# Performance work log

Hardware: AMD Instinct MI355X
Metric: run time of the kernel (lower is better)

Reference implementation:

```python
import jax, jax.numpy as jnp
import numpy as np

B, S, D = 8, 1024, 1152
H = 16
HD = D // H
HID = int(D * 4.0)
LN_EPS = 1e-5


def layer_norm(x, w, b):
    m = jnp.mean(x, axis=-1, keepdims=True)
    v = jnp.mean(jnp.square(x - m), axis=-1, keepdims=True)
    return (x - m) * jax.lax.rsqrt(v + LN_EPS) * w + b


def modulate(x, shift, scale):
    # shift/scale: [B, D] broadcast over seq
    return x * (1.0 + scale[:, None, :]) + shift[:, None, :]


def setup_inputs() -> dict:
    key = jax.random.key(0)
    ks = jax.random.split(key, 16)
    s = 0.02
    return {
        "x": jax.random.normal(ks[0], (B, S, D), jnp.float32),
        "c": jax.random.normal(ks[1], (B, D), jnp.float32),
        "ln1_w": jnp.ones((D,), jnp.float32),
        "ln1_b": jnp.zeros((D,), jnp.float32),
        "wq": jax.random.normal(ks[2], (D, D), jnp.float32) * s,
        "wk": jax.random.normal(ks[3], (D, D), jnp.float32) * s,
        "wv": jax.random.normal(ks[4], (D, D), jnp.float32) * s,
        "wo": jax.random.normal(ks[5], (D, D), jnp.float32) * s,
        "wo_b": jnp.zeros((D,), jnp.float32),
        "ln2_w": jnp.ones((D,), jnp.float32),
        "ln2_b": jnp.zeros((D,), jnp.float32),
        "fc1_w": jax.random.normal(ks[6], (D, HID), jnp.float32) * s,
        "fc1_b": jnp.zeros((HID,), jnp.float32),
        "fc2_w": jax.random.normal(ks[7], (HID, D), jnp.float32) * s,
        "fc2_b": jnp.zeros((D,), jnp.float32),
        "ada_w": jax.random.normal(ks[8], (D, 6 * D), jnp.float32) * s,
        "ada_b": jnp.zeros((6 * D,), jnp.float32),
    }


def attention(x, wq, wk, wv, wo, wo_b):
    b, s, d = x.shape
    q = (x @ wq).reshape(b, s, H, HD).transpose(0, 2, 1, 3)  # [B,H,S,hd]
    k = (x @ wk).reshape(b, s, H, HD).transpose(0, 2, 1, 3)
    v = (x @ wv).reshape(b, s, H, HD).transpose(0, 2, 1, 3)
    scale = 1.0 / np.sqrt(HD).astype(np.float32)
    att = jnp.einsum("bhqd,bhkd->bhqk", q, k) * scale
    att = jax.nn.softmax(att, axis=-1)
    out = jnp.einsum("bhqk,bhkd->bhqd", att, v)
    out = out.transpose(0, 2, 1, 3).reshape(b, s, d)
    return out @ wo + wo_b


def reference(x, c, ln1_w, ln1_b, wq, wk, wv, wo, wo_b, ln2_w, ln2_b,
              fc1_w, fc1_b, fc2_w, fc2_b, ada_w, ada_b):
    mod = jax.nn.silu(c) @ ada_w + ada_b  # [B, 6D]
    sh_msa, sc_msa, g_msa, sh_mlp, sc_mlp, g_mlp = jnp.split(mod, 6, axis=1)
    h = modulate(layer_norm(x, ln1_w, ln1_b), sh_msa, sc_msa)
    x = x + g_msa[:, None, :] * attention(h, wq, wk, wv, wo, wo_b)
    h = modulate(layer_norm(x, ln2_w, ln2_b), sh_mlp, sc_mlp)
    h = jax.nn.gelu(h @ fc1_w + fc1_b, approximate=False) @ fc2_w + fc2_b
    x = x + g_mlp[:, None, :] * h
    return x
```

## Files before the change

kernel.cpp:

```cpp
#include <hip/hip_runtime.h>
#include <hip/hip_bf16.h>


typedef unsigned short u16;
typedef unsigned int u32;
typedef __attribute__((ext_vector_type(8))) short bf16x8;
typedef __attribute__((ext_vector_type(4))) float f32x4;
typedef __attribute__((ext_vector_type(16))) float f32x16;

#define MFMA16(a, b, c) __builtin_amdgcn_mfma_f32_16x16x32_bf16((a), (b), (c), 0, 0, 0)
#define MFMA32(a, b, c) __builtin_amdgcn_mfma_f32_32x32x16_bf16((a), (b), (c), 0, 0, 0)

__device__ __forceinline__ u16 f2bf(float f) {
  __hip_bfloat16 h = __float2bfloat16(f);
  return __builtin_bit_cast(u16, h);
}

__device__ __forceinline__ float bf2f(u16 u) {
  u32 v = ((u32)u) << 16;
  return __builtin_bit_cast(float, v);
}

__device__ __forceinline__ void gload16(const u16* g, u16* l) {
  __builtin_amdgcn_global_load_lds(
      (const __attribute__((address_space(1))) unsigned int*)(const void*)g,
      (__attribute__((address_space(3))) unsigned int*)(void*)l, 16, 0, 0);
}

__global__ __launch_bounds__(256) void k_modproj1(const float* __restrict__ cc,
                                                  const float* __restrict__ aw,
                                                  float* __restrict__ partial) {
  __shared__ float lc[8][144];
  int kc = blockIdx.y;
  for (int i = threadIdx.x; i < 1152; i += 256) {
    int b = i / 144, k = i % 144;
    float v = cc[b * 1152 + kc * 144 + k];
    lc[b][k] = v / (1.f + __expf(-v));
  }
  __syncthreads();
  int j = blockIdx.x * 256 + threadIdx.x;
  float acc[8] = {0, 0, 0, 0, 0, 0, 0, 0};
  for (int k = 0; k < 144; ++k) {
    float w = aw[(size_t)(kc * 144 + k) * 6912 + j];
    #pragma unroll
    for (int b = 0; b < 8; ++b) acc[b] += lc[b][k] * w;
  }
  #pragma unroll
  for (int b = 0; b < 8; ++b) partial[((size_t)kc * 8 + b) * 6912 + j] = acc[b];
}

__global__ __launch_bounds__(256) void k_modproj2(const float* __restrict__ partial,
                                                  const float* __restrict__ ab,
                                                  float* __restrict__ mo) {
  int j = blockIdx.x * 256 + threadIdx.x;
  float bias = ab[j];
  #pragma unroll
  for (int b = 0; b < 8; ++b) {
    float s = 0.f;
    #pragma unroll
    for (int kc = 0; kc < 8; ++kc) s += partial[((size_t)kc * 8 + b) * 6912 + j];
    mo[(size_t)b * 6912 + j] = s + bias;
  }
}

__global__ __launch_bounds__(256) void k_tcvt(const float* __restrict__ in, u16* __restrict__ out,
                                              int K, int N) {
  __shared__ float t[32][33];
  int tx = threadIdx.x & 31, ty = threadIdx.x >> 5;
  size_t bx = (size_t)blockIdx.x * 32, by = (size_t)blockIdx.y * 32;
  #pragma unroll
  for (int i = 0; i < 4; ++i) t[ty + 8 * i][tx] = in[(by + ty + 8 * i) * N + bx + tx];
  __syncthreads();
  #pragma unroll
  for (int i = 0; i < 4; ++i) out[(bx + ty + 8 * i) * K + by + tx] = f2bf(t[tx][ty + 8 * i]);
}

__global__ __launch_bounds__(256) void k_lnmod(const float* __restrict__ xin,
                                               const float* __restrict__ w,
                                               const float* __restrict__ bs,
                                               const float* __restrict__ mo,
                                               int sh_off, int sc_off, u16* __restrict__ o) {
  int row = blockIdx.x;
  int b = row >> 10;
  int tid = threadIdx.x;
  const float4* x4 = (const float4*)(xin + (size_t)row * 1152);
  float4 v0 = x4[tid];
  float4 v1 = make_float4(0.f, 0.f, 0.f, 0.f);
  if (tid < 32) v1 = x4[256 + tid];
  float s = v0.x + v0.y + v0.z + v0.w + v1.x + v1.y + v1.z + v1.w;
  float sq = v0.x * v0.x + v0.y * v0.y + v0.z * v0.z + v0.w * v0.w +
             v1.x * v1.x + v1.y * v1.y + v1.z * v1.z + v1.w * v1.w;
  #pragma unroll
  for (int d = 32; d > 0; d >>= 1) { s += __shfl_down(s, d); sq += __shfl_down(sq, d); }
  __shared__ float ps[4], pq[4];
  int wid = tid >> 6, lane = tid & 63;
  if (lane == 0) { ps[wid] = s; pq[wid] = sq; }
  __syncthreads();
  float S = ps[0] + ps[1] + ps[2] + ps[3];
  float SQ = pq[0] + pq[1] + pq[2] + pq[3];
  float mean = S * (1.f / 1152.f);
  float var = SQ * (1.f / 1152.f) - mean * mean;
  float rs = rsqrtf(var + 1e-5f);
  const float* shp = mo + (size_t)b * 6912 + sh_off;
  const float* scp = mo + (size_t)b * 6912 + sc_off;
  u16* orow = o + (size_t)row * 1152;
  {
    int col = 4 * tid;
    ushort4 u; float y;
    y = (v0.x - mean) * rs * w[col + 0] + bs[col + 0]; u.x = f2bf(y * (1.f + scp[col + 0]) + shp[col + 0]);
    y = (v0.y - mean) * rs * w[col + 1] + bs[col + 1]; u.y = f2bf(y * (1.f + scp[col + 1]) + shp[col + 1]);
    y = (v0.z - mean) * rs * w[col + 2] + bs[col + 2]; u.z = f2bf(y * (1.f + scp[col + 2]) + shp[col + 2]);
    y = (v0.w - mean) * rs * w[col + 3] + bs[col + 3]; u.w = f2bf(y * (1.f + scp[col + 3]) + shp[col + 3]);
    *(ushort4*)&orow[col] = u;
  }
  if (tid < 32) {
    int col = 1024 + 4 * tid;
    ushort4 u; float y;
    y = (v1.x - mean) * rs * w[col + 0] + bs[col + 0]; u.x = f2bf(y * (1.f + scp[col + 0]) + shp[col + 0]);
    y = (v1.y - mean) * rs * w[col + 1] + bs[col + 1]; u.y = f2bf(y * (1.f + scp[col + 1]) + shp[col + 1]);
    y = (v1.z - mean) * rs * w[col + 2] + bs[col + 2]; u.z = f2bf(y * (1.f + scp[col + 2]) + shp[col + 2]);
    y = (v1.w - mean) * rs * w[col + 3] + bs[col + 3]; u.w = f2bf(y * (1.f + scp[col + 3]) + shp[col + 3]);
    *(ushort4*)&orow[col] = u;
  }
}

template <int EPI>
__global__ __launch_bounds__(512, 2) void k_gemm8p(const u16* __restrict__ A,
                                                   const u16* __restrict__ Bt,
                                                   int Kst, int klen,
                                                   u16* __restrict__ Cb,
                                                   const float* __restrict__ bias,
                                                   u16* __restrict__ vt) {
  const int tid = threadIdx.x;
  const int w = tid >> 6, lane = tid & 63;
  const int wm = w >> 2, wn = w & 3;
  const int l31 = lane & 31, hi = lane >> 5;

  const int nwg = gridDim.x * gridDim.y;
  const int id = blockIdx.y * gridDim.x + blockIdx.x;
  const int swz = (id & 7) * (nwg >> 3) + (id >> 3);
  const int tM = (swz / gridDim.x) * 256, tN = (swz % gridDim.x) * 256;
  const int koff = blockIdx.z * klen;

  __shared__ u16 lA[2][2][256 * 32];
  __shared__ u16 lB[2][2][256 * 32];
  f32x16 acc[4][2];
  #pragma unroll
  for (int m = 0; m < 4; ++m)
    #pragma unroll
    for (int n = 0; n < 2; ++n)
      #pragma unroll
      for (int r = 0; r < 16; ++r) acc[m][n][r] = 0.f;

  const int lrow = lane >> 2, lseg = lane & 3;
  const int fl = (lrow & 3) ^ ((lrow >> 2) & 3);
  const u16* gA = A + (size_t)(tM + w * 32 + lrow) * Kst + (lseg ^ fl) * 8 + koff;
  const u16* gB = Bt + (size_t)(tN + w * 32 + lrow) * Kst + (lseg ^ fl) * 8 + koff;
  const size_t rstep = (size_t)16 * Kst;
  const int wo0 = (w * 32) * 32, wo1 = (w * 32 + 16) * 32;
  const int fr = (l31 & 3) ^ ((l31 >> 2) & 3);
  const int c0 = (hi ^ fr) * 8;
  const int c1 = ((hi ^ fr) ^ 2) * 8;
  const int arow = (wm * 128 + l31) * 32;
  const int brow = (wn * 64 + l31) * 32;

#define SA(BUF, KH, KO)                                       \
  do {                                                        \
    gload16(gA + (KO), &lA[BUF][KH][wo0]);                    \
    gload16(gA + rstep + (KO), &lA[BUF][KH][wo1]);            \
  } while (0)
#define SB(BUF, KH, KO)                                       \
  do {                                                        \
    gload16(gB + (KO), &lB[BUF][KH][wo0]);                    \
    gload16(gB + rstep + (KO), &lB[BUF][KH][wo1]);            \
  } while (0)
#define VM(Nst) asm volatile("s_waitcnt vmcnt(" #Nst ")" ::: "memory")

#define PHASE(CB, KH, PM, STAGE_STMT)                                            \
  do {                                                                           \
    __builtin_amdgcn_s_barrier();                                                \
    __builtin_amdgcn_sched_barrier(0);                                           \
    bf16x8 a0_ = *(const bf16x8*)&lA[CB][KH][arow + (2 * (PM)) * 1024 + c0];     \
    bf16x8 a1_ = *(const bf16x8*)&lA[CB][KH][arow + (2 * (PM)) * 1024 + c1];     \
    bf16x8 a2_ = *(const bf16x8*)&lA[CB][KH][arow + (2 * (PM) + 1) * 1024 + c0]; \
    bf16x8 a3_ = *(const bf16x8*)&lA[CB][KH][arow + (2 * (PM) + 1) * 1024 + c1]; \
    bf16x8 b0_ = *(const bf16x8*)&lB[CB][KH][brow + c0];                         \
    bf16x8 b1_ = *(const bf16x8*)&lB[CB][KH][brow + c1];                         \
    bf16x8 b2_ = *(const bf16x8*)&lB[CB][KH][brow + 1024 + c0];                  \
    bf16x8 b3_ = *(const bf16x8*)&lB[CB][KH][brow + 1024 + c1];                  \
    STAGE_STMT;                                                                  \
    asm volatile("s_waitcnt lgkmcnt(0)" ::: "memory");                           \
    __builtin_amdgcn_sched_barrier(0);                                           \
    __builtin_amdgcn_s_setprio(1);                                               \
    acc[2 * (PM)][0]     = MFMA32(a0_, b0_, acc[2 * (PM)][0]);                   \
    acc[2 * (PM)][1]     = MFMA32(a0_, b2_, acc[2 * (PM)][1]);                   \
    acc[2 * (PM) + 1][0] = MFMA32(a2_, b0_, acc[2 * (PM) + 1][0]);               \
    acc[2 * (PM) + 1][1] = MFMA32(a2_, b2_, acc[2 * (PM) + 1][1]);               \
    acc[2 * (PM)][0]     = MFMA32(a1_, b1_, acc[2 * (PM)][0]);                   \
    acc[2 * (PM)][1]     = MFMA32(a1_, b3_, acc[2 * (PM)][1]);                   \
    acc[2 * (PM) + 1][0] = MFMA32(a3_, b1_, acc[2 * (PM) + 1][0]);               \
    acc[2 * (PM) + 1][1] = MFMA32(a3_, b3_, acc[2 * (PM) + 1][1]);               \
    __builtin_amdgcn_s_setprio(0);                                               \
  } while (0)

  const int NIT = klen >> 7;
  SA(0, 0, 0); SB(0, 0, 0); SA(0, 1, 32); SB(0, 1, 32); SA(1, 0, 64);
  for (int it = 0; it < NIT - 1; ++it) {
    const int kb = it * 128;
    VM(6); PHASE(0, 0, 0, SB(1, 0, kb + 64));
           PHASE(0, 0, 1, SA(1, 1, kb + 96));
    VM(6); PHASE(0, 1, 0, SB(1, 1, kb + 96));
           PHASE(0, 1, 1, SA(0, 0, kb + 128));
    VM(6); PHASE(1, 0, 0, SB(0, 0, kb + 128));
           PHASE(1, 0, 1, SA(0, 1, kb + 160));
    VM(6); PHASE(1, 1, 0, SB(0, 1, kb + 160));
           PHASE(1, 1, 1, SA(1, 0, kb + 192));
  }
  {
    const int kb = (NIT - 1) * 128;
    VM(6); PHASE(0, 0, 0, SB(1, 0, kb + 64));
           PHASE(0, 0, 1, SA(1, 1, kb + 96));
    VM(6); PHASE(0, 1, 0, SB(1, 1, kb + 96));
           PHASE(0, 1, 1, (void)0);
    VM(4); PHASE(1, 0, 0, (void)0);
           PHASE(1, 0, 1, (void)0);
    VM(0); PHASE(1, 1, 0, (void)0);
           PHASE(1, 1, 1, (void)0);
  }
#undef SA
#undef SB
#undef VM
#undef PHASE

  #pragma unroll
  for (int m = 0; m < 4; ++m)
    #pragma unroll
    for (int n = 0; n < 2; ++n) {
      int gcol = tN + wn * 64 + n * 32 + l31;
      #pragma unroll
      for (int q = 0; q < 4; ++q) {
        int grow0 = tM + wm * 128 + m * 32 + hi * 4 + q * 8;
        if (EPI == 3) {
          if (gcol < 2304) {
            #pragma unroll
            for (int r = 0; r < 4; ++r)
              Cb[(size_t)(grow0 + r) * 3456 + gcol] = f2bf(acc[m][n][q * 4 + r]);
          } else if (gcol < 3456) {
            int qq = gcol - 2304;
            int hh = qq / 72;
            int d = qq - hh * 72;
            int bb = grow0 >> 10, sl = grow0 & 1023;
            ushort4 u;
            u.x = f2bf(acc[m][n][q * 4 + 0]); u.y = f2bf(acc[m][n][q * 4 + 1]);
            u.z = f2bf(acc[m][n][q * 4 + 2]); u.w = f2bf(acc[m][n][q * 4 + 3]);
            *(ushort4*)&vt[(((size_t)bb * 16 + hh) * 72 + d) * 1024 + sl] = u;
          }
        } else if (EPI == 5) {
          if (gcol < 1152) {
            u16* Po = Cb + (size_t)blockIdx.z * 9437184ull;
            #pragma unroll
            for (int r = 0; r < 4; ++r)
              Po[(size_t)(grow0 + r) * 1152 + gcol] = f2bf(acc[m][n][q * 4 + r]);
          }
        } else {
          const int NC = gridDim.x * 256;
          float bi = bias[gcol];
          #pragma unroll
          for (int r = 0; r < 4; ++r) {
            float z = acc[m][n][q * 4 + r] + bi;
            float z2 = z * z;
            float u = z * __fmaf_rn(z2, -0.0713548162f, -1.5957691216f);
            float e = __expf(u);
            Cb[(size_t)(grow0 + r) * NC + gcol] = f2bf(z * __builtin_amdgcn_rcpf(1.f + e));
          }
        }
      }
    }
}

template <int EPI>
__global__ __launch_bounds__(256) void k_gemm(const u16* __restrict__ A, const u16* __restrict__ Bt,
                                              int Kst, int klen, u16* __restrict__ Cb,
                                              float* __restrict__ Cf,
                                              const float* __restrict__ bias,
                                              const float* __restrict__ res,
                                              const float* __restrict__ mo, int goff,
                                              u16* __restrict__ vt) {
  const int tid = threadIdx.x;
  const int w = tid >> 6, lane = tid & 63;
  const int wr = w >> 1, wc = w & 1;
  const int l31 = lane & 31, hi = lane >> 5;

  const int nwg = gridDim.x * gridDim.y;
  const int id = blockIdx.y * gridDim.x + blockIdx.x;
  const int swz = (id & 7) * (nwg >> 3) + (id >> 3);
  const int tM = (swz / gridDim.x) * 128, tN = (swz % gridDim.x) * 128;
  const int N = gridDim.x * 128;
  const int koff = blockIdx.z * klen;

  __shared__ u16 lA[3][128 * 32];
  __shared__ u16 lB[3][128 * 32];
  f32x16 acc[2][2];
  #pragma unroll
  for (int m = 0; m < 2; ++m)
    #pragma unroll
    for (int n = 0; n < 2; ++n)
      #pragma unroll
      for (int r = 0; r < 16; ++r) acc[m][n][r] = 0.f;

  const int lrow = lane >> 2, lseg = lane & 3;
  const int fl = (lrow & 3) ^ ((lrow >> 2) & 3);
  const u16* gA = A + (size_t)(tM + w * 32 + lrow) * Kst + (lseg ^ fl) * 8 + koff;
  const u16* gB = Bt + (size_t)(tN + w * 32 + lrow) * Kst + (lseg ^ fl) * 8 + koff;
  const size_t rstep = (size_t)16 * Kst;
  const int wo0 = (w * 32) * 32, wo1 = (w * 32 + 16) * 32;
  const int fr = (l31 & 3) ^ ((l31 >> 2) & 3);
  const int c0 = (hi ^ fr) * 8;
  const int c1 = ((hi ^ fr) ^ 2) * 8;
  const int arow = (wr * 64 + l31) * 32;
  const int brow = (wc * 64 + l31) * 32;

#define STAGE(buf, ks)                        \
  do {                                        \
    gload16(gA + (ks), lA[buf] + wo0);        \
    gload16(gA + rstep + (ks), lA[buf] + wo1);\
    gload16(gB + (ks), lB[buf] + wo0);        \
    gload16(gB + rstep + (ks), lB[buf] + wo1);\
  } while (0)

#define COMPUTE(buf)                                                            \
  do {                                                                          \
    bf16x8 a00 = *(const bf16x8*)&lA[buf][arow + c0];                           \
    bf16x8 a01 = *(const bf16x8*)&lA[buf][arow + c1];                           \
    bf16x8 a10 = *(const bf16x8*)&lA[buf][arow + 1024 + c0];                    \
    bf16x8 a11 = *(const bf16x8*)&lA[buf][arow + 1024 + c1];                    \
    bf16x8 b00 = *(const bf16x8*)&lB[buf][brow + c0];                           \
    bf16x8 b01 = *(const bf16x8*)&lB[buf][brow + c1];                           \
    bf16x8 b10 = *(const bf16x8*)&lB[buf][brow + 1024 + c0];                    \
    bf16x8 b11 = *(const bf16x8*)&lB[buf][brow + 1024 + c1];                    \
    __builtin_amdgcn_s_setprio(1);                                              \
    acc[0][0] = MFMA32(a00, b00, acc[0][0]);                                    \
    acc[0][1] = MFMA32(a00, b10, acc[0][1]);                                    \
    acc[1][0] = MFMA32(a10, b00, acc[1][0]);                                    \
    acc[1][1] = MFMA32(a10, b10, acc[1][1]);                                    \
    acc[0][0] = MFMA32(a01, b01, acc[0][0]);                                    \
    acc[0][1] = MFMA32(a01, b11, acc[0][1]);                                    \
    acc[1][0] = MFMA32(a11, b01, acc[1][0]);                                    \
    acc[1][1] = MFMA32(a11, b11, acc[1][1]);                                    \
    __builtin_amdgcn_s_setprio(0);                                              \
  } while (0)

#define WAITBAR(Nst)                                          \
  do {                                                        \
    asm volatile("s_waitcnt vmcnt(" #Nst ")" ::: "memory");   \
    __builtin_amdgcn_s_barrier();                             \
    __builtin_amdgcn_sched_barrier(0);                        \
  } while (0)

  const int nt = klen >> 5;
  STAGE(0, 0);
  STAGE(1, 32);
  int ks = 64;
  for (int g = 0; g < nt / 3 - 1; ++g) {
    WAITBAR(4); STAGE(2, ks);      COMPUTE(0);
    WAITBAR(4); STAGE(0, ks + 32); COMPUTE(1);
    WAITBAR(4); STAGE(1, ks + 64); COMPUTE(2);
    ks += 96;
  }
  WAITBAR(4); STAGE(2, ks); COMPUTE(0);
  WAITBAR(4); COMPUTE(1);
  WAITBAR(0); COMPUTE(2);
#undef STAGE
#undef COMPUTE
#undef WAITBAR

  #pragma unroll
  for (int m = 0; m < 2; ++m)
    #pragma unroll
    for (int n = 0; n < 2; ++n) {
      int gcol = tN + wc * 64 + n * 32 + l31;
      #pragma unroll
      for (int q = 0; q < 4; ++q) {
        int grow0 = tM + wr * 64 + m * 32 + hi * 4 + q * 8;
        float g = mo[(size_t)(grow0 >> 10) * 6912 + goff + gcol];
        float bi = bias[gcol];
        #pragma unroll
        for (int r = 0; r < 4; ++r) {
          size_t idx = (size_t)(grow0 + r) * N + gcol;
          Cf[idx] = res[idx] + g * (acc[m][n][q * 4 + r] + bi);
        }
      }
    }
}

__global__ __launch_bounds__(256) void k_fc2red(const u16* __restrict__ p,
                                                const float* __restrict__ x1,
                                                const float* __restrict__ bias,
                                                const float* __restrict__ mo,
                                                float* __restrict__ out) {
  size_t i = ((size_t)blockIdx.x * 256 + threadIdx.x) * 4;
  int row = (int)(i / 1152);
  int col = (int)(i - (size_t)row * 1152);
  int b = row >> 10;
  ushort4 a0 = *(const ushort4*)(p + i);
  ushort4 a1 = *(const ushort4*)(p + 9437184ull + i);
  ushort4 a2 = *(const ushort4*)(p + 18874368ull + i);
  float4 r = *(const float4*)(x1 + i);
  const float* gp = mo + (size_t)b * 6912 + 5760 + col;
  const float* bp = bias + col;
  float4 o;
  o.x = r.x + gp[0] * (bf2f(a0.x) + bf2f(a1.x) + bf2f(a2.x) + bp[0]);
  o.y = r.y + gp[1] * (bf2f(a0.y) + bf2f(a1.y) + bf2f(a2.y) + bp[1]);
  o.z = r.z + gp[2] * (bf2f(a0.z) + bf2f(a1.z) + bf2f(a2.z) + bp[2]);
  o.w = r.w + gp[3] * (bf2f(a0.w) + bf2f(a1.w) + bf2f(a2.w) + bp[3]);
  *(float4*)(out + i) = o;
}

__global__ __launch_bounds__(256) void k_attn(const u16* __restrict__ QKV, const u16* __restrict__ Vt,
                                              u16* __restrict__ O) {
  const int tid = threadIdx.x;
  const int w = tid >> 6, lane = tid & 63;
  const int lr = lane & 15, kg = lane >> 4;
  int bx = blockIdx.x;
  bx = (bx & 7) * 256 + (bx >> 3);
  const int qt = bx & 15, h = (bx >> 4) & 15, b = bx >> 8;

  __shared__ u16 lQ[64][104];
  __shared__ u16 lK[64][104];
  __shared__ u16 lVt[80][72];
  __shared__ u16 lPt[4][16][72];

  const size_t qkbase = (size_t)b * 1024 * 3456 + (size_t)h * 72;
  const u16* Qg = QKV + qkbase;
  const u16* Kg = QKV + qkbase + 1152;
  const u16* Vg = Vt + ((size_t)(b * 16 + h) * 72) * 1024;

  const uint4 z4 = make_uint4(0, 0, 0, 0);
  for (int L = tid; L < 192; L += 256) {
    int r = L / 3, s = L - (L / 3) * 3;
    *(uint4*)&lQ[r][72 + s * 8] = z4;
    *(uint4*)&lK[r][72 + s * 8] = z4;
  }
  for (int L = tid; L < 72; L += 256) {
    int r = L / 9, s = L - (L / 9) * 9;
    *(uint4*)&lVt[72 + r][s * 8] = z4;
  }
  {
    int L = tid; int r = L / 9, s = L - r * 9;
    *(uint4*)&lQ[r][s * 8] = *(const uint4*)(Qg + (size_t)(qt * 64 + r) * 3456 + s * 8);
    L = tid + 256; r = L / 9; s = L - r * 9;
    *(uint4*)&lQ[r][s * 8] = *(const uint4*)(Qg + (size_t)(qt * 64 + r) * 3456 + s * 8);
    if (tid < 64) {
      L = tid + 512; r = L / 9; s = L - r * 9;
      *(uint4*)&lQ[r][s * 8] = *(const uint4*)(Qg + (size_t)(qt * 64 + r) * 3456 + s * 8);
    }
  }
  __syncthreads();

  bf16x8 bq[3];
  #pragma unroll
  for (int ks = 0; ks < 3; ++ks) bq[ks] = *(const bf16x8*)&lQ[w * 16 + lr][ks * 32 + kg * 8];

  const float scale = 0.11785113019775793f;
  float mrun = -1e30f, lrun = 0.f;
  f32x4 oacc[5];
  #pragma unroll
  for (int nd = 0; nd < 5; ++nd) oacc[nd] = f32x4{0.f, 0.f, 0.f, 0.f};

  for (int kt = 0; kt < 16; ++kt) {
    __syncthreads();
    {
      int L = tid; int r = L / 9, s = L - (L / 9) * 9;
      *(uint4*)&lK[r][s * 8] = *(const uint4*)(Kg + (size_t)(kt * 64 + r) * 3456 + s * 8);
      int d = tid >> 3, sg = tid & 7;
      *(uint4*)&lVt[d][sg * 8] = *(const uint4*)(Vg + (size_t)d * 1024 + kt * 64 + sg * 8);
      L = tid + 256; r = L / 9; s = L - r * 9;
      *(uint4*)&lK[r][s * 8] = *(const uint4*)(Kg + (size_t)(kt * 64 + r) * 3456 + s * 8);
      d = (tid + 256) >> 3; sg = tid & 7;
      *(uint4*)&lVt[d][sg * 8] = *(const uint4*)(Vg + (size_t)d * 1024 + kt * 64 + sg * 8);
      if (tid < 64) {
        L = tid + 512; r = L / 9; s = L - r * 9;
        *(uint4*)&lK[r][s * 8] = *(const uint4*)(Kg + (size_t)(kt * 64 + r) * 3456 + s * 8);
        d = (tid + 512) >> 3;
        *(uint4*)&lVt[d][sg * 8] = *(const uint4*)(Vg + (size_t)d * 1024 + kt * 64 + sg * 8);
      }
    }
    __syncthreads();

    f32x4 sfr[4];
    __builtin_amdgcn_s_setprio(1);
    #pragma unroll
    for (int kb = 0; kb < 4; ++kb) {
      f32x4 sv = f32x4{0.f, 0.f, 0.f, 0.f};
      #pragma unroll
      for (int ks = 0; ks < 3; ++ks) {
        bf16x8 ak = *(const bf16x8*)&lK[kb * 16 + lr][ks * 32 + kg * 8];
        sv = MFMA16(ak, bq[ks], sv);
      }
      sfr[kb] = sv;
    }
    __builtin_amdgcn_s_setprio(0);

    float mx = sfr[0][0];
    #pragma unroll
    for (int kb = 0; kb < 4; ++kb)
      #pragma unroll
      for (int r = 0; r < 4; ++r) mx = fmaxf(mx, sfr[kb][r]);
    mx = fmaxf(mx, __shfl_xor(mx, 16));
    mx = fmaxf(mx, __shfl_xor(mx, 32));
    mx *= scale;
    float mn = fmaxf(mrun, mx);
    float al = __expf(mrun - mn);
    mrun = mn;
    float sum = 0.f;
    #pragma unroll
    for (int kb = 0; kb < 4; ++kb) {
      #pragma unroll
      for (int rp = 0; rp < 2; ++rp) {
        float p0 = __expf(__fmaf_rn(sfr[kb][2 * rp], scale, -mn));
        float p1 = __expf(__fmaf_rn(sfr[kb][2 * rp + 1], scale, -mn));
        sum += p0 + p1;
        u32 pk = (u32)f2bf(p0) | ((u32)f2bf(p1) << 16);
        *(u32*)&lPt[w][lr][kb * 16 + kg * 4 + rp * 2] = pk;
      }
    }
    sum += __shfl_xor(sum, 16);
    sum += __shfl_xor(sum, 32);
    lrun = lrun * al + sum;
    #pragma unroll
    for (int nd = 0; nd < 5; ++nd)
      #pragma unroll
      for (int r = 0; r < 4; ++r) oacc[nd][r] *= al;

    __builtin_amdgcn_s_setprio(1);
    #pragma unroll
    for (int s = 0; s < 2; ++s) {
      bf16x8 bp = *(const bf16x8*)&lPt[w][lr][s * 32 + kg * 8];
      #pragma unroll
      for (int nd = 0; nd < 5; ++nd) {
        bf16x8 av = *(const bf16x8*)&lVt[nd * 16 + lr][s * 32 + kg * 8];
        oacc[nd] = MFMA16(av, bp, oacc[nd]);
      }
    }
    __builtin_amdgcn_s_setprio(0);
  }

  float inv = 1.f / lrun;
  size_t orow = ((size_t)b * 1024 + qt * 64 + w * 16 + lr) * 1152 + h * 72;
  #pragma unroll
  for (int nd = 0; nd < 5; ++nd) {
    int d0 = nd * 16 + kg * 4;
    if (d0 < 72) {
      ushort4 u;
      u.x = f2bf(oacc[nd][0] * inv);
      u.y = f2bf(oacc[nd][1] * inv);
      u.z = f2bf(oacc[nd][2] * inv);
      u.w = f2bf(oacc[nd][3] * inv);
      *(ushort4*)&O[orow + d0] = u;
    }
  }
}

extern "C" void kernel_launch(void* const* d_in, const int* in_sizes, int n_in,
                              void* d_out, int out_size, void* d_ws, size_t ws_size,
                              hipStream_t stream) {
  const float* x     = (const float*)d_in[0];
  const float* c     = (const float*)d_in[1];
  const float* ln1_w = (const float*)d_in[2];
  const float* ln1_b = (const float*)d_in[3];
  const float* wq    = (const float*)d_in[4];
  const float* wk    = (const float*)d_in[5];
  const float* wv    = (const float*)d_in[6];
  const float* wo    = (const float*)d_in[7];
  const float* wo_b  = (const float*)d_in[8];
  const float* ln2_w = (const float*)d_in[9];
  const float* ln2_b = (const float*)d_in[10];
  const float* fc1_w = (const float*)d_in[11];
  const float* fc1_b = (const float*)d_in[12];
  const float* fc2_w = (const float*)d_in[13];
  const float* fc2_b = (const float*)d_in[14];
  const float* ada_w = (const float*)d_in[15];
  const float* ada_b = (const float*)d_in[16];
  float* out = (float*)d_out;

  char* base = (char*)d_ws;
  size_t off = 0;
  auto alloc = [&](size_t nbytes) -> void* {
    void* p = base + off;
    off += (nbytes + 255) & ~(size_t)255;
    return p;
  };
  const size_t MD = 8192ull * 1152;
  float* partial = (float*)alloc(64ull * 6912 * 4);
  float* modb   = (float*)alloc(55296 * 4);
  u16* qkvT = (u16*)alloc(3584ull * 1152 * 2);
  u16* woT  = (u16*)alloc(1152ull * 1152 * 2);
  u16* fc1T = (u16*)alloc(4608ull * 1152 * 2);
  u16* fc2T = (u16*)alloc(1280ull * 4608 * 2);
  u16* hbuf = (u16*)alloc(MD * 2);
  float* x1 = (float*)alloc(MD * 4);
  u16* vtb  = (u16*)alloc(128ull * 72 * 1024 * 2);
  u16* fc2p = (u16*)alloc(3ull * MD * 2);
  u16* big  = (u16*)alloc(8192ull * 4608 * 2);
  u16* qkv = big;
  u16* m1 = big;

  k_modproj1<<<dim3(27, 8), 256, 0, stream>>>(c, ada_w, partial);
  k_modproj2<<<27, 256, 0, stream>>>(partial, ada_b, modb);
  k_tcvt<<<dim3(36, 36), 256, 0, stream>>>(wq, qkvT, 1152, 1152);
  k_tcvt<<<dim3(36, 36), 256, 0, stream>>>(wk, qkvT + 1152ull * 1152, 1152, 1152);
  k_tcvt<<<dim3(36, 36), 256, 0, stream>>>(wv, qkvT + 2304ull * 1152, 1152, 1152);
  k_tcvt<<<dim3(36, 36), 256, 0, stream>>>(wo, woT, 1152, 1152);
  k_tcvt<<<dim3(144, 36), 256, 0, stream>>>(fc1_w, fc1T, 1152, 4608);
  k_tcvt<<<dim3(36, 144), 256, 0, stream>>>(fc2_w, fc2T, 4608, 1152);

  k_lnmod<<<8192, 256, 0, stream>>>(x, ln1_w, ln1_b, modb, 0, 1152, hbuf);
  k_gemm8p<3><<<dim3(14, 32), 512, 0, stream>>>(hbuf, qkvT, 1152, 1152, qkv, nullptr, vtb);
  k_attn<<<2048, 256, 0, stream>>>(qkv, vtb, hbuf);
  k_gemm<1><<<dim3(9, 64), 256, 0, stream>>>(hbuf, woT, 1152, 1152, nullptr, x1, wo_b, x, modb, 2304, nullptr);
  k_lnmod<<<8192, 256, 0, stream>>>(x1, ln2_w, ln2_b, modb, 3456, 4608, hbuf);
  k_gemm8p<2><<<dim3(18, 32), 512, 0, stream>>>(hbuf, fc1T, 1152, 1152, m1, fc1_b, nullptr);
  k_gemm8p<5><<<dim3(5, 32, 3), 512, 0, stream>>>(m1, fc2T, 4608, 1536, fc2p, nullptr, nullptr);
  k_fc2red<<<9216, 256, 0, stream>>>(fc2p, x1, fc2_b, modb, out);
}
```

Measured before the change: 558.7 us.

## Merge half-phases into full 4x2 MFMA phases with deeper A/B prefetch

Each GEMM pipeline phase now loads all four A fragments and both B fragments and issues sixteen MFMAs, instead of splitting the work into two half-phases with a barrier between them. This halves the number of s_barrier and lgkmcnt waits per k-step. The prologue now issues one more B stage ahead, and the vmcnt waits change to match. In exchange, more fragment registers are live at once, and each phase's global load group becomes larger and less evenly spread between MFMA blocks.

```diff
diff --git a/kernel.cpp b/kernel.cpp
--- a/kernel.cpp
+++ b/kernel.cpp
@@ -176,56 +176,55 @@
   } while (0)
 #define VM(Nst) asm volatile("s_waitcnt vmcnt(" #Nst ")" ::: "memory")
 
-#define PHASE(CB, KH, PM, STAGE_STMT)                                            \
-  do {                                                                           \
-    __builtin_amdgcn_s_barrier();                                                \
-    __builtin_amdgcn_sched_barrier(0);                                           \
-    bf16x8 a0_ = *(const bf16x8*)&lA[CB][KH][arow + (2 * (PM)) * 1024 + c0];     \
-    bf16x8 a1_ = *(const bf16x8*)&lA[CB][KH][arow + (2 * (PM)) * 1024 + c1];     \
-    bf16x8 a2_ = *(const bf16x8*)&lA[CB][KH][arow + (2 * (PM) + 1) * 1024 + c0]; \
-    bf16x8 a3_ = *(const bf16x8*)&lA[CB][KH][arow + (2 * (PM) + 1) * 1024 + c1]; \
-    bf16x8 b0_ = *(const bf16x8*)&lB[CB][KH][brow + c0];                         \
-    bf16x8 b1_ = *(const bf16x8*)&lB[CB][KH][brow + c1];                         \
-    bf16x8 b2_ = *(const bf16x8*)&lB[CB][KH][brow + 1024 + c0];                  \
-    bf16x8 b3_ = *(const bf16x8*)&lB[CB][KH][brow + 1024 + c1];                  \
-    STAGE_STMT;                                                                  \
-    asm volatile("s_waitcnt lgkmcnt(0)" ::: "memory");                           \
-    __builtin_amdgcn_sched_barrier(0);                                           \
-    __builtin_amdgcn_s_setprio(1);                                               \
-    acc[2 * (PM)][0]     = MFMA32(a0_, b0_, acc[2 * (PM)][0]);                   \
-    acc[2 * (PM)][1]     = MFMA32(a0_, b2_, acc[2 * (PM)][1]);                   \
-    acc[2 * (PM) + 1][0] = MFMA32(a2_, b0_, acc[2 * (PM) + 1][0]);               \
-    acc[2 * (PM) + 1][1] = MFMA32(a2_, b2_, acc[2 * (PM) + 1][1]);               \
-    acc[2 * (PM)][0]     = MFMA32(a1_, b1_, acc[2 * (PM)][0]);                   \
-    acc[2 * (PM)][1]     = MFMA32(a1_, b3_, acc[2 * (PM)][1]);                   \
-    acc[2 * (PM) + 1][0] = MFMA32(a3_, b1_, acc[2 * (PM) + 1][0]);               \
-    acc[2 * (PM) + 1][1] = MFMA32(a3_, b3_, acc[2 * (PM) + 1][1]);               \
-    __builtin_amdgcn_s_setprio(0);                                               \
+#define PHASE(CB, KH, STAGE_STMT)                                               \
+  do {                                                                          \
+    __builtin_amdgcn_s_barrier();                                               \
+    __builtin_amdgcn_sched_barrier(0);                                          \
+    bf16x8 af[4][2], bf[2][2];                                                  \
+    _Pragma("unroll")                                                           \
+    for (int m_ = 0; m_ < 4; ++m_) {                                            \
+      af[m_][0] = *(const bf16x8*)&lA[CB][KH][arow + m_ * 1024 + c0];           \
+      af[m_][1] = *(const bf16x8*)&lA[CB][KH][arow + m_ * 1024 + c1];           \
+    }                                                                           \
+    _Pragma("unroll")                                                           \
+    for (int n_ = 0; n_ < 2; ++n_) {                                            \
+      bf[n_][0] = *(const bf16x8*)&lB[CB][KH][brow + n_ * 1024 + c0];           \
+      bf[n_][1] = *(const bf16x8*)&lB[CB][KH][brow + n_ * 1024 + c1];           \
+    }                                                                           \
+    STAGE_STMT;                                                                 \
+    asm volatile("s_waitcnt lgkmcnt(0)" ::: "memory");                          \
+    __builtin_amdgcn_sched_barrier(0);                                          \
+    __builtin_amdgcn_s_setprio(1);                                              \
+    _Pragma("unroll")                                                           \
+    for (int m_ = 0; m_ < 4; ++m_)                                              \
+      _Pragma("unroll")                                                         \
+      for (int n_ = 0; n_ < 2; ++n_)                                            \
+        acc[m_][n_] = MFMA32(af[m_][0], bf[n_][0], acc[m_][n_]);                \
+    _Pragma("unroll")                                                           \
+    for (int m_ = 0; m_ < 4; ++m_)                                              \
+      _Pragma("unroll")                                                         \
+      for (int n_ = 0; n_ < 2; ++n_)                                            \
+        acc[m_][n_] = MFMA32(af[m_][1], bf[n_][1], acc[m_][n_]);                \
+    __builtin_amdgcn_s_setprio(0);                                              \
   } while (0)
 
   const int NIT = klen >> 7;
-  SA(0, 0, 0); SB(0, 0, 0); SA(0, 1, 32); SB(0, 1, 32); SA(1, 0, 64);
+  SA(0, 0, 0); SB(0, 0, 0);
+  SA(0, 1, 32); SB(0, 1, 32);
+  SA(1, 0, 64); SB(1, 0, 64);
   for (int it = 0; it < NIT - 1; ++it) {
     const int kb = it * 128;
-    VM(6); PHASE(0, 0, 0, SB(1, 0, kb + 64));
-           PHASE(0, 0, 1, SA(1, 1, kb + 96));
-    VM(6); PHASE(0, 1, 0, SB(1, 1, kb + 96));
-           PHASE(0, 1, 1, SA(0, 0, kb + 128));
-    VM(6); PHASE(1, 0, 0, SB(0, 0, kb + 128));
-           PHASE(1, 0, 1, SA(0, 1, kb + 160));
-    VM(6); PHASE(1, 1, 0, SB(0, 1, kb + 160));
-           PHASE(1, 1, 1, SA(1, 0, kb + 192));
+    VM(8); PHASE(0, 0, { SA(1, 1, kb + 96);  SB(1, 1, kb + 96);  });
+    VM(8); PHASE(0, 1, { SA(0, 0, kb + 128); SB(0, 0, kb + 128); });
+    VM(8); PHASE(1, 0, { SA(0, 1, kb + 160); SB(0, 1, kb + 160); });
+    VM(8); PHASE(1, 1, { SA(1, 0, kb + 192); SB(1, 0, kb + 192); });
   }
   {
     const int kb = (NIT - 1) * 128;
-    VM(6); PHASE(0, 0, 0, SB(1, 0, kb + 64));
-           PHASE(0, 0, 1, SA(1, 1, kb + 96));
-    VM(6); PHASE(0, 1, 0, SB(1, 1, kb + 96));
-           PHASE(0, 1, 1, (void)0);
-    VM(4); PHASE(1, 0, 0, (void)0);
-           PHASE(1, 0, 1, (void)0);
-    VM(0); PHASE(1, 1, 0, (void)0);
-           PHASE(1, 1, 1, (void)0);
+    VM(8); PHASE(0, 0, { SA(1, 1, kb + 96); SB(1, 1, kb + 96); });
+    VM(8); PHASE(0, 1, (void)0);
+    VM(4); PHASE(1, 0, (void)0);
+    VM(0); PHASE(1, 1, (void)0);
   }
 #undef SA
 #undef SB
```

New measurement: 539.2 us. -3.5%, faster.
